# Kernel optimization log

Measured on AMD Instinct MI355X. Metric: run time of the kernel, lower is better.

Reference implementation:

```python
import jax, jax.numpy as jnp
import numpy as np

B, S, D, H = 2, 2048, 1024, 16
HD = D // H
SCALE = float(np.sqrt(HD))


def setup_inputs() -> dict:
    key = jax.random.key(0)
    ks = jax.random.split(key, 11)
    mk = lambda k, shape, s=0.02: (jax.random.normal(k, shape, dtype=jnp.float32) * s)
    query = jax.random.normal(ks[0], (B, S, D), dtype=jnp.float32)
    key_t = jax.random.normal(ks[1], (B, S, D), dtype=jnp.float32)
    value = jax.random.normal(ks[2], (B, S, D), dtype=jnp.float32)
    # causal mask: True = position is masked out
    mask = jnp.triu(jnp.ones((S, S), dtype=bool), k=1)
    return {
        "query": query, "key": key_t, "value": value, "mask": mask,
        "Wq": mk(ks[3], (D, D)), "bq": jnp.zeros((D,), jnp.float32),
        "Wk": mk(ks[4], (D, D)), "bk": jnp.zeros((D,), jnp.float32),
        "Wv": mk(ks[5], (D, D)), "bv": jnp.zeros((D,), jnp.float32),
        "Wo": mk(ks[6], (D, D)), "bo": jnp.zeros((D,), jnp.float32),
    }


def reference(query, key, value, mask, Wq, bq, Wk, bk, Wv, bv, Wo, bo):
    b = query.shape[0]
    # projections; nn.Linear computes x @ W.T + b
    q = (query @ Wq.T + bq).reshape(b, -1, H, HD).transpose(0, 2, 1, 3)  # (b,h,sq,hd)
    k = (key @ Wk.T + bk).reshape(b, -1, H, HD).transpose(0, 2, 1, 3)    # (b,h,sk,hd)
    v = (value @ Wv.T + bv).reshape(b, -1, H, HD).transpose(0, 2, 1, 3)  # (b,h,sk,hd)
    scores = jnp.einsum("bhqd,bhkd->bhqk", q, k) / SCALE
    scores = jnp.where(mask[None, None, :, :], -jnp.inf, scores)
    attn_weights = jax.nn.softmax(scores, axis=-1)  # (b,h,sq,sk)
    # dropout is identity in eval mode
    attn_out = jnp.einsum("bhqk,bhkd->bhqd", attn_weights, v)
    attn_out = attn_out.transpose(0, 2, 1, 3).reshape(b, -1, D)
    output = attn_out @ Wo.T + bo
    return output, attn_weights
```

## Files before the change

kernel.cpp:

```cpp
#include <hip/hip_runtime.h>

typedef __bf16 bf16;
typedef __bf16 bf16_8 __attribute__((ext_vector_type(8)));
typedef __bf16 bf16_4 __attribute__((ext_vector_type(4)));
typedef float f32x4 __attribute__((ext_vector_type(4)));

constexpr int kB = 2, kS = 2048, kD = 1024, kH = 16, kHD = 64;
constexpr int kM = kB * kS;
constexpr float kInvScale = 0.125f;

#define GLOBAL_AS const __attribute__((address_space(1)))
#define LDS_AS __attribute__((address_space(3)))

__device__ __forceinline__ void async_copy16(const bf16* g, bf16* l) {
  __builtin_amdgcn_global_load_lds((GLOBAL_AS unsigned int*)g,
                                   (LDS_AS unsigned int*)l, 16, 0, 0);
}

__global__ __launch_bounds__(256) void cvt4(const float4* __restrict__ src,
                                            bf16* __restrict__ dst, int n4) {
  int i = blockIdx.x * blockDim.x + threadIdx.x;
  if (i >= n4) return;
  float4 v = src[i];
  bf16_4 o = {(bf16)v.x, (bf16)v.y, (bf16)v.z, (bf16)v.w};
  *(bf16_4*)(dst + (size_t)i * 4) = o;
}

__device__ __forceinline__ void gemm_core(const bf16* __restrict__ A,
                                          const bf16* __restrict__ Bm,
                                          int m0, int n0,
                                          bf16* ldsA, bf16* ldsB,
                                          f32x4 acc[4][4]) {
  const int t = threadIdx.x;
  const int lane = t & 63, wave = t >> 6;
  const int l16 = lane & 15, quad = lane >> 4;
  const int wm = (wave >> 1) * 64, wn = (wave & 1) * 64;
  const f32x4 z4 = {0.f, 0.f, 0.f, 0.f};
#pragma unroll
  for (int i = 0; i < 4; ++i)
#pragma unroll
    for (int j = 0; j < 4; ++j) acc[i][j] = z4;

  for (int kt = 0; kt < kD; kt += 32) {
#pragma unroll
    for (int rep = 0; rep < 2; ++rep) {
      int q = t + rep * 256;
      int row = q >> 2, cc = q & 3;
      bf16* lbase_a = ldsA + (size_t)(wave * 64 + rep * 256) * 8;
      bf16* lbase_b = ldsB + (size_t)(wave * 64 + rep * 256) * 8;
      async_copy16(A + (size_t)(m0 + row) * kD + kt + cc * 8, lbase_a);
      async_copy16(Bm + (size_t)(n0 + row) * kD + kt + cc * 8, lbase_b);
    }
    __syncthreads();
    bf16_8 af[4], bfr[4];
#pragma unroll
    for (int i = 0; i < 4; ++i)
      af[i] = *(const bf16_8*)(ldsA + (wm + i * 16 + l16) * 32 + quad * 8);
#pragma unroll
    for (int j = 0; j < 4; ++j)
      bfr[j] = *(const bf16_8*)(ldsB + (wn + j * 16 + l16) * 32 + quad * 8);
#pragma unroll
    for (int i = 0; i < 4; ++i)
#pragma unroll
      for (int j = 0; j < 4; ++j)
        acc[i][j] = __builtin_amdgcn_mfma_f32_16x16x32_bf16(af[i], bfr[j],
                                                            acc[i][j], 0, 0, 0);
    __syncthreads();
  }
}

__global__ __launch_bounds__(256) void gemm_qkv(
    const bf16* __restrict__ qb, const bf16* __restrict__ kb,
    const bf16* __restrict__ vb, const bf16* __restrict__ wq,
    const bf16* __restrict__ wk, const bf16* __restrict__ wv,
    const float* __restrict__ bq, const float* __restrict__ bk,
    const float* __restrict__ bv, bf16* __restrict__ Qh,
    bf16* __restrict__ Kh, bf16* __restrict__ Vh) {
  __shared__ __align__(16) bf16 ldsA[128 * 32];
  __shared__ __align__(16) bf16 ldsB[128 * 32];
  const bf16 *A, *W;
  const float* bias;
  bf16* Out;
  int z = blockIdx.z;
  if (z == 0) { A = qb; W = wq; bias = bq; Out = Qh; }
  else if (z == 1) { A = kb; W = wk; bias = bk; Out = Kh; }
  else { A = vb; W = wv; bias = bv; Out = Vh; }
  int m0 = blockIdx.x * 128, n0 = blockIdx.y * 128;
  f32x4 acc[4][4];
  gemm_core(A, W, m0, n0, ldsA, ldsB, acc);

  const int t = threadIdx.x, lane = t & 63, wave = t >> 6;
  const int l16 = lane & 15, quad = lane >> 4;
  const int wm = (wave >> 1) * 64, wn = (wave & 1) * 64;
#pragma unroll
  for (int i = 0; i < 4; ++i)
#pragma unroll
    for (int j = 0; j < 4; ++j)
#pragma unroll
      for (int r = 0; r < 4; ++r) {
        int m = m0 + wm + i * 16 + quad * 4 + r;
        int n = n0 + wn + j * 16 + l16;
        float v = acc[i][j][r] + bias[n];
        int b = m >> 11, s = m & (kS - 1);
        int h = n >> 6, hd = n & 63;
        Out[((size_t)(b * kH + h) * kS + s) * kHD + hd] = (bf16)v;
      }
}

__global__ __launch_bounds__(256) void gemm_out(const bf16* __restrict__ AO,
                                                const bf16* __restrict__ wo,
                                                const float* __restrict__ bo,
                                                float* __restrict__ Cout) {
  __shared__ __align__(16) bf16 ldsA[128 * 32];
  __shared__ __align__(16) bf16 ldsB[128 * 32];
  int m0 = blockIdx.x * 128, n0 = blockIdx.y * 128;
  f32x4 acc[4][4];
  gemm_core(AO, wo, m0, n0, ldsA, ldsB, acc);

  const int t = threadIdx.x, lane = t & 63, wave = t >> 6;
  const int l16 = lane & 15, quad = lane >> 4;
  const int wm = (wave >> 1) * 64, wn = (wave & 1) * 64;
#pragma unroll
  for (int i = 0; i < 4; ++i)
#pragma unroll
    for (int j = 0; j < 4; ++j)
#pragma unroll
      for (int r = 0; r < 4; ++r) {
        int m = m0 + wm + i * 16 + quad * 4 + r;
        int n = n0 + wn + j * 16 + l16;
        Cout[(size_t)m * kD + n] = acc[i][j][r] + bo[n];
      }
}

__global__ __launch_bounds__(256) void attn_kernel(
    const bf16* __restrict__ Qh, const bf16* __restrict__ Kh,
    const bf16* __restrict__ Vh, float* __restrict__ attnW,
    bf16* __restrict__ AO) {
  __shared__ __align__(16) bf16 ldsK[64 * 64];
  __shared__ __align__(16) bf16 ldsVt[64 * 72];
  __shared__ __align__(16) bf16 ldsP[4 * 16 * 64];

  const int t = threadIdx.x, lane = t & 63, wave = t >> 6;
  const int l16 = lane & 15, quad = lane >> 4;
  const int qt = blockIdx.x, bh = blockIdx.y;
  const int q0 = qt * 64;

  const bf16* Qbase = Qh + ((size_t)bh * kS + q0) * kHD;
  const bf16* Kbase = Kh + (size_t)bh * kS * kHD;
  const bf16* Vbase = Vh + (size_t)bh * kS * kHD;

  bf16_8 aq0 = *(const bf16_8*)(Qbase + (wave * 16 + l16) * kHD + quad * 8);
  bf16_8 aq1 = *(const bf16_8*)(Qbase + (wave * 16 + l16) * kHD + 32 + quad * 8);

  float m_i[4], l_i[4];
#pragma unroll
  for (int r = 0; r < 4; ++r) { m_i[r] = -3.0e38f; l_i[r] = 0.f; }

  for (int kt = 0; kt <= qt; ++kt) {
    const int k0 = kt * 64;
#pragma unroll
    for (int rep = 0; rep < 2; ++rep) {
      int q = t + rep * 256;
      async_copy16(Kbase + (size_t)(k0 + (q >> 3)) * kHD + (q & 7) * 8,
                   ldsK + (size_t)(wave * 64 + rep * 256) * 8);
    }
    __syncthreads();
    f32x4 sacc[4];
#pragma unroll
    for (int j = 0; j < 4; ++j) {
      bf16_8 b0 = *(const bf16_8*)(ldsK + (j * 16 + l16) * 64 + quad * 8);
      bf16_8 b1 = *(const bf16_8*)(ldsK + (j * 16 + l16) * 64 + 32 + quad * 8);
      f32x4 z = {0.f, 0.f, 0.f, 0.f};
      z = __builtin_amdgcn_mfma_f32_16x16x32_bf16(aq0, b0, z, 0, 0, 0);
      z = __builtin_amdgcn_mfma_f32_16x16x32_bf16(aq1, b1, z, 0, 0, 0);
      sacc[j] = z;
    }
#pragma unroll
    for (int j = 0; j < 4; ++j)
#pragma unroll
      for (int r = 0; r < 4; ++r) {
        int qrow = q0 + wave * 16 + quad * 4 + r;
        int kcol = k0 + j * 16 + l16;
        float v = sacc[j][r] * kInvScale;
        sacc[j][r] = (kcol > qrow) ? -3.0e38f : v;
      }
#pragma unroll
    for (int r = 0; r < 4; ++r) {
      float mx = fmaxf(fmaxf(sacc[0][r], sacc[1][r]),
                       fmaxf(sacc[2][r], sacc[3][r]));
#pragma unroll
      for (int off = 1; off < 16; off <<= 1) mx = fmaxf(mx, __shfl_xor(mx, off, 64));
      float mnew = fmaxf(m_i[r], mx);
      float sum = 0.f;
#pragma unroll
      for (int j = 0; j < 4; ++j) sum += __expf(sacc[j][r] - mnew);
#pragma unroll
      for (int off = 1; off < 16; off <<= 1) sum += __shfl_xor(sum, off, 64);
      l_i[r] = l_i[r] * __expf(m_i[r] - mnew) + sum;
      m_i[r] = mnew;
    }
    __syncthreads();
  }

  float rl[4];
#pragma unroll
  for (int r = 0; r < 4; ++r) rl[r] = 1.0f / l_i[r];

  const f32x4 z4 = {0.f, 0.f, 0.f, 0.f};
  f32x4 oacc[4];
#pragma unroll
  for (int d = 0; d < 4; ++d) oacc[d] = z4;

  for (int kt = 0; kt < kS / 64; ++kt) {
    const int k0 = kt * 64;
    if (kt > qt) {
      const float4 zf = {0.f, 0.f, 0.f, 0.f};
      int row = t >> 2;
      float* dst = attnW + ((size_t)bh * kS + q0 + row) * kS + k0 + (t & 3) * 16;
#pragma unroll
      for (int f = 0; f < 4; ++f) ((float4*)dst)[f] = zf;
      continue;
    }
#pragma unroll
    for (int rep = 0; rep < 2; ++rep) {
      int q = t + rep * 256;
      async_copy16(Kbase + (size_t)(k0 + (q >> 3)) * kHD + (q & 7) * 8,
                   ldsK + (size_t)(wave * 64 + rep * 256) * 8);
    }
    {
      int d = t & 63, kk0 = (t >> 6) * 16;
#pragma unroll
      for (int i = 0; i < 16; ++i)
        ldsVt[(size_t)d * 72 + kk0 + i] =
            Vbase[(size_t)(k0 + kk0 + i) * kHD + d];
    }
    __syncthreads();
    f32x4 sacc[4];
#pragma unroll
    for (int j = 0; j < 4; ++j) {
      bf16_8 b0 = *(const bf16_8*)(ldsK + (j * 16 + l16) * 64 + quad * 8);
      bf16_8 b1 = *(const bf16_8*)(ldsK + (j * 16 + l16) * 64 + 32 + quad * 8);
      f32x4 z = {0.f, 0.f, 0.f, 0.f};
      z = __builtin_amdgcn_mfma_f32_16x16x32_bf16(aq0, b0, z, 0, 0, 0);
      z = __builtin_amdgcn_mfma_f32_16x16x32_bf16(aq1, b1, z, 0, 0, 0);
      sacc[j] = z;
    }
#pragma unroll
    for (int j = 0; j < 4; ++j)
#pragma unroll
      for (int r = 0; r < 4; ++r) {
        int qrl = wave * 16 + quad * 4 + r;
        int qrow = q0 + qrl;
        int kcol = k0 + j * 16 + l16;
        float v = sacc[j][r] * kInvScale;
        float p = (kcol > qrow) ? 0.f : __expf(v - m_i[r]) * rl[r];
        attnW[((size_t)bh * kS + qrow) * kS + kcol] = p;
        ldsP[(size_t)qrl * 64 + j * 16 + l16] = (bf16)p;
      }
    __syncthreads();
    bf16_8 ap0 = *(const bf16_8*)(ldsP + (wave * 16 + l16) * 64 + quad * 8);
    bf16_8 ap1 = *(const bf16_8*)(ldsP + (wave * 16 + l16) * 64 + 32 + quad * 8);
#pragma unroll
    for (int dsub = 0; dsub < 4; ++dsub) {
      bf16_8 bv0 = *(const bf16_8*)(ldsVt + (dsub * 16 + l16) * 72 + quad * 8);
      bf16_8 bv1 = *(const bf16_8*)(ldsVt + (dsub * 16 + l16) * 72 + 32 + quad * 8);
      oacc[dsub] = __builtin_amdgcn_mfma_f32_16x16x32_bf16(ap0, bv0, oacc[dsub], 0, 0, 0);
      oacc[dsub] = __builtin_amdgcn_mfma_f32_16x16x32_bf16(ap1, bv1, oacc[dsub], 0, 0, 0);
    }
    __syncthreads();
  }

  const int b = bh >> 4, h = bh & 15;
#pragma unroll
  for (int dsub = 0; dsub < 4; ++dsub)
#pragma unroll
    for (int r = 0; r < 4; ++r) {
      int qrow = q0 + wave * 16 + quad * 4 + r;
      int d = dsub * 16 + l16;
      AO[((size_t)(b * kS + qrow)) * kD + h * kHD + d] = (bf16)oacc[dsub][r];
    }
}

extern "C" void kernel_launch(void* const* d_in, const int* in_sizes, int n_in,
                              void* d_out, int out_size, void* d_ws, size_t ws_size,
                              hipStream_t stream) {
  const float* query = (const float*)d_in[0];
  const float* key_t = (const float*)d_in[1];
  const float* value = (const float*)d_in[2];
  const float* Wq = (const float*)d_in[4];
  const float* bq = (const float*)d_in[5];
  const float* Wk = (const float*)d_in[6];
  const float* bk = (const float*)d_in[7];
  const float* Wv = (const float*)d_in[8];
  const float* bv = (const float*)d_in[9];
  const float* Wo = (const float*)d_in[10];
  const float* bo = (const float*)d_in[11];

  float* out = (float*)d_out;
  float* attnW = out + (size_t)kM * kD;

  bf16* qb = (bf16*)d_ws;
  bf16* kb = qb + (size_t)kM * kD;
  bf16* vb = kb + (size_t)kM * kD;
  bf16* Qh = vb + (size_t)kM * kD;
  bf16* Kh = Qh + (size_t)kM * kD;
  bf16* Vh = Kh + (size_t)kM * kD;
  bf16* AO = Vh + (size_t)kM * kD;
  bf16* wqb = AO + (size_t)kM * kD;
  bf16* wkb = wqb + (size_t)kD * kD;
  bf16* wvb = wkb + (size_t)kD * kD;
  bf16* wob = wvb + (size_t)kD * kD;

  const int n4_x = kM * kD / 4;
  const int n4_w = kD * kD / 4;
  cvt4<<<n4_x / 256, 256, 0, stream>>>((const float4*)query, qb, n4_x);
  cvt4<<<n4_x / 256, 256, 0, stream>>>((const float4*)key_t, kb, n4_x);
  cvt4<<<n4_x / 256, 256, 0, stream>>>((const float4*)value, vb, n4_x);
  cvt4<<<n4_w / 256, 256, 0, stream>>>((const float4*)Wq, wqb, n4_w);
  cvt4<<<n4_w / 256, 256, 0, stream>>>((const float4*)Wk, wkb, n4_w);
  cvt4<<<n4_w / 256, 256, 0, stream>>>((const float4*)Wv, wvb, n4_w);
  cvt4<<<n4_w / 256, 256, 0, stream>>>((const float4*)Wo, wob, n4_w);

  gemm_qkv<<<dim3(kM / 128, kD / 128, 3), 256, 0, stream>>>(
      qb, kb, vb, wqb, wkb, wvb, bq, bk, bv, Qh, Kh, Vh);

  attn_kernel<<<dim3(kS / 64, kB * kH), 256, 0, stream>>>(Qh, Kh, Vh, attnW, AO);

  gemm_out<<<dim3(kM / 128, kD / 128), 256, 0, stream>>>(AO, wob, bo, out);
}
```

Before: 803.5 us.

## Restructure attention with double-buffered K/V, pre-transposed V and max-free softmax

Attention now double-buffers K and V tiles in LDS via async copies. V is pre-transposed by a separate kernel, replacing the scalar strided V gather. The 1/sqrt(d) scale is folded into the Q projection, and the online running max is dropped, so the first pass only accumulates exp sums. Query tiles are launched heaviest-first for causal load balance, and the seven conversion launches are merged into two. Dropping the max subtraction risks exp overflow when scores are large, and the transpose adds a kernel and extra workspace.

```diff
diff --git a/kernel.cpp b/kernel.cpp
--- a/kernel.cpp
+++ b/kernel.cpp
@@ -7,7 +7,7 @@
 
 constexpr int kB = 2, kS = 2048, kD = 1024, kH = 16, kHD = 64;
 constexpr int kM = kB * kS;
-constexpr float kInvScale = 0.125f;
+constexpr int kNT = kS / 64;
 
 #define GLOBAL_AS const __attribute__((address_space(1)))
 #define LDS_AS __attribute__((address_space(3)))
@@ -17,12 +17,33 @@
                                    (LDS_AS unsigned int*)l, 16, 0, 0);
 }
 
-__global__ __launch_bounds__(256) void cvt4(const float4* __restrict__ src,
-                                            bf16* __restrict__ dst, int n4) {
-  int i = blockIdx.x * blockDim.x + threadIdx.x;
-  if (i >= n4) return;
-  float4 v = src[i];
-  bf16_4 o = {(bf16)v.x, (bf16)v.y, (bf16)v.z, (bf16)v.w};
+__device__ __forceinline__ void barrier_lgkm() {
+  asm volatile("s_waitcnt lgkmcnt(0)\n\ts_barrier" ::: "memory");
+}
+
+__global__ __launch_bounds__(256) void cvt_act(
+    const float4* __restrict__ q, const float4* __restrict__ k,
+    const float4* __restrict__ v, bf16* __restrict__ oq,
+    bf16* __restrict__ ok, bf16* __restrict__ ov) {
+  const float4* src = blockIdx.y == 0 ? q : blockIdx.y == 1 ? k : v;
+  bf16* dst = blockIdx.y == 0 ? oq : blockIdx.y == 1 ? ok : ov;
+  int i = blockIdx.x * 256 + threadIdx.x;
+  float4 x = src[i];
+  bf16_4 o = {(bf16)x.x, (bf16)x.y, (bf16)x.z, (bf16)x.w};
+  *(bf16_4*)(dst + (size_t)i * 4) = o;
+}
+
+__global__ __launch_bounds__(256) void cvt_w(
+    const float4* __restrict__ a, const float4* __restrict__ b,
+    const float4* __restrict__ c, const float4* __restrict__ d,
+    bf16* __restrict__ oa, bf16* __restrict__ ob, bf16* __restrict__ oc,
+    bf16* __restrict__ od) {
+  int z = blockIdx.y;
+  const float4* src = z == 0 ? a : z == 1 ? b : z == 2 ? c : d;
+  bf16* dst = z == 0 ? oa : z == 1 ? ob : z == 2 ? oc : od;
+  int i = blockIdx.x * 256 + threadIdx.x;
+  float4 x = src[i];
+  bf16_4 o = {(bf16)x.x, (bf16)x.y, (bf16)x.z, (bf16)x.w};
   *(bf16_4*)(dst + (size_t)i * 4) = o;
 }
 
@@ -85,6 +106,7 @@
   if (z == 0) { A = qb; W = wq; bias = bq; Out = Qh; }
   else if (z == 1) { A = kb; W = wk; bias = bk; Out = Kh; }
   else { A = vb; W = wv; bias = bv; Out = Vh; }
+  const float scale = (z == 0) ? 0.125f : 1.0f;
   int m0 = blockIdx.x * 128, n0 = blockIdx.y * 128;
   f32x4 acc[4][4];
   gemm_core(A, W, m0, n0, ldsA, ldsB, acc);
@@ -100,11 +122,34 @@
       for (int r = 0; r < 4; ++r) {
         int m = m0 + wm + i * 16 + quad * 4 + r;
         int n = n0 + wn + j * 16 + l16;
-        float v = acc[i][j][r] + bias[n];
+        float v = (acc[i][j][r] + bias[n]) * scale;
         int b = m >> 11, s = m & (kS - 1);
         int h = n >> 6, hd = n & 63;
         Out[((size_t)(b * kH + h) * kS + s) * kHD + hd] = (bf16)v;
       }
+}
+
+__global__ __launch_bounds__(256) void transpose_v(const bf16* __restrict__ Vh,
+                                                   bf16* __restrict__ Vt) {
+  __shared__ bf16 tile[64][72];
+  const int t = threadIdx.x;
+  const int s0 = blockIdx.x * 64, bh = blockIdx.y;
+#pragma unroll
+  for (int it = 0; it < 2; ++it) {
+    int chunk = t + it * 256;
+    int s = chunk >> 3, d0 = (chunk & 7) * 8;
+    bf16_8 v = *(const bf16_8*)(Vh + ((size_t)bh * kS + s0 + s) * kHD + d0);
+#pragma unroll
+    for (int j = 0; j < 8; ++j) tile[d0 + j][s] = v[j];
+  }
+  __syncthreads();
+#pragma unroll
+  for (int it = 0; it < 2; ++it) {
+    int chunk = t + it * 256;
+    int d = chunk >> 3, c0 = (chunk & 7) * 8;
+    bf16_8 o = *(const bf16_8*)&tile[d][c0];
+    *(bf16_8*)(Vt + ((size_t)bh * kHD + d) * kS + s0 + c0) = o;
+  }
 }
 
 __global__ __launch_bounds__(256) void gemm_out(const bf16* __restrict__ AO,
@@ -134,42 +179,64 @@
 
 __global__ __launch_bounds__(256) void attn_kernel(
     const bf16* __restrict__ Qh, const bf16* __restrict__ Kh,
-    const bf16* __restrict__ Vh, float* __restrict__ attnW,
+    const bf16* __restrict__ Vt, float* __restrict__ attnW,
     bf16* __restrict__ AO) {
-  __shared__ __align__(16) bf16 ldsK[64 * 64];
-  __shared__ __align__(16) bf16 ldsVt[64 * 72];
-  __shared__ __align__(16) bf16 ldsP[4 * 16 * 64];
+  __shared__ __align__(16) bf16 ldsK[2][64 * 64];
+  __shared__ __align__(16) bf16 ldsV[2][64 * 64];
+  __shared__ __align__(16) bf16 ldsP[64 * 64];
 
   const int t = threadIdx.x, lane = t & 63, wave = t >> 6;
   const int l16 = lane & 15, quad = lane >> 4;
-  const int qt = blockIdx.x, bh = blockIdx.y;
+  const int bh = blockIdx.x;
+  const int qt = (kNT - 1) - blockIdx.y;
   const int q0 = qt * 64;
 
   const bf16* Qbase = Qh + ((size_t)bh * kS + q0) * kHD;
   const bf16* Kbase = Kh + (size_t)bh * kS * kHD;
-  const bf16* Vbase = Vh + (size_t)bh * kS * kHD;
+  const bf16* Vtbase = Vt + (size_t)bh * kHD * kS;
 
   bf16_8 aq0 = *(const bf16_8*)(Qbase + (wave * 16 + l16) * kHD + quad * 8);
   bf16_8 aq1 = *(const bf16_8*)(Qbase + (wave * 16 + l16) * kHD + 32 + quad * 8);
 
-  float m_i[4], l_i[4];
-#pragma unroll
-  for (int r = 0; r < 4; ++r) { m_i[r] = -3.0e38f; l_i[r] = 0.f; }
-
+  const int dq = t >> 3, dc = (t & 7) * 8;
+#define ISSUE_K(kt, buf)                                                      \
+  {                                                                           \
+    const int k0_ = (kt) * 64;                                                \
+    async_copy16(Kbase + (size_t)(k0_ / 64 * 64 + dq) * kHD + dc,             \
+                 &ldsK[buf][(size_t)(wave * 64) * 8]);                        \
+    async_copy16(Kbase + (size_t)(k0_ + ((t + 256) >> 3)) * kHD +             \
+                     (((t + 256) & 7) * 8),                                   \
+                 &ldsK[buf][(size_t)(wave * 64 + 256) * 8]);                  \
+  }
+#define ISSUE_V(kt, buf)                                                      \
+  {                                                                           \
+    const int k0_ = (kt) * 64;                                                \
+    async_copy16(Vtbase + (size_t)dq * kS + k0_ + dc,                         \
+                 &ldsV[buf][(size_t)(wave * 64) * 8]);                        \
+    async_copy16(Vtbase + (size_t)((t + 256) >> 3) * kS + k0_ +               \
+                     (((t + 256) & 7) * 8),                                   \
+                 &ldsV[buf][(size_t)(wave * 64 + 256) * 8]);                  \
+  }
+
+  float lp[4] = {0.f, 0.f, 0.f, 0.f};
+  {
+    const int k0f = 0;
+    async_copy16(Kbase + (size_t)(k0f + dq) * kHD + dc,
+                 &ldsK[0][(size_t)(wave * 64) * 8]);
+    async_copy16(Kbase + (size_t)(k0f + ((t + 256) >> 3)) * kHD +
+                     (((t + 256) & 7) * 8),
+                 &ldsK[0][(size_t)(wave * 64 + 256) * 8]);
+  }
   for (int kt = 0; kt <= qt; ++kt) {
+    __syncthreads();
+    if (kt < qt) ISSUE_K(kt + 1, (kt + 1) & 1);
+    const bf16* Kl = ldsK[kt & 1];
     const int k0 = kt * 64;
-#pragma unroll
-    for (int rep = 0; rep < 2; ++rep) {
-      int q = t + rep * 256;
-      async_copy16(Kbase + (size_t)(k0 + (q >> 3)) * kHD + (q & 7) * 8,
-                   ldsK + (size_t)(wave * 64 + rep * 256) * 8);
-    }
-    __syncthreads();
     f32x4 sacc[4];
 #pragma unroll
     for (int j = 0; j < 4; ++j) {
-      bf16_8 b0 = *(const bf16_8*)(ldsK + (j * 16 + l16) * 64 + quad * 8);
-      bf16_8 b1 = *(const bf16_8*)(ldsK + (j * 16 + l16) * 64 + 32 + quad * 8);
+      bf16_8 b0 = *(const bf16_8*)(Kl + (j * 16 + l16) * 64 + quad * 8);
+      bf16_8 b1 = *(const bf16_8*)(Kl + (j * 16 + l16) * 64 + 32 + quad * 8);
       f32x4 z = {0.f, 0.f, 0.f, 0.f};
       z = __builtin_amdgcn_mfma_f32_16x16x32_bf16(aq0, b0, z, 0, 0, 0);
       z = __builtin_amdgcn_mfma_f32_16x16x32_bf16(aq1, b1, z, 0, 0, 0);
@@ -181,65 +248,40 @@
       for (int r = 0; r < 4; ++r) {
         int qrow = q0 + wave * 16 + quad * 4 + r;
         int kcol = k0 + j * 16 + l16;
-        float v = sacc[j][r] * kInvScale;
-        sacc[j][r] = (kcol > qrow) ? -3.0e38f : v;
+        lp[r] += (kcol > qrow) ? 0.f : __expf(sacc[j][r]);
       }
-#pragma unroll
-    for (int r = 0; r < 4; ++r) {
-      float mx = fmaxf(fmaxf(sacc[0][r], sacc[1][r]),
-                       fmaxf(sacc[2][r], sacc[3][r]));
-#pragma unroll
-      for (int off = 1; off < 16; off <<= 1) mx = fmaxf(mx, __shfl_xor(mx, off, 64));
-      float mnew = fmaxf(m_i[r], mx);
-      float sum = 0.f;
-#pragma unroll
-      for (int j = 0; j < 4; ++j) sum += __expf(sacc[j][r] - mnew);
-#pragma unroll
-      for (int off = 1; off < 16; off <<= 1) sum += __shfl_xor(sum, off, 64);
-      l_i[r] = l_i[r] * __expf(m_i[r] - mnew) + sum;
-      m_i[r] = mnew;
-    }
-    __syncthreads();
-  }
-
+  }
   float rl[4];
 #pragma unroll
-  for (int r = 0; r < 4; ++r) rl[r] = 1.0f / l_i[r];
+  for (int r = 0; r < 4; ++r) {
+    float s = lp[r];
+#pragma unroll
+    for (int off = 1; off < 16; off <<= 1) s += __shfl_xor(s, off, 64);
+    rl[r] = 1.0f / s;
+  }
 
   const f32x4 z4 = {0.f, 0.f, 0.f, 0.f};
   f32x4 oacc[4];
 #pragma unroll
   for (int d = 0; d < 4; ++d) oacc[d] = z4;
 
-  for (int kt = 0; kt < kS / 64; ++kt) {
+  __syncthreads();
+  ISSUE_K(0, 0);
+  ISSUE_V(0, 0);
+  for (int kt = 0; kt <= qt; ++kt) {
+    __syncthreads();
+    if (kt < qt) {
+      ISSUE_K(kt + 1, (kt + 1) & 1);
+      ISSUE_V(kt + 1, (kt + 1) & 1);
+    }
+    const bf16* Kl = ldsK[kt & 1];
+    const bf16* Vl = ldsV[kt & 1];
     const int k0 = kt * 64;
-    if (kt > qt) {
-      const float4 zf = {0.f, 0.f, 0.f, 0.f};
-      int row = t >> 2;
-      float* dst = attnW + ((size_t)bh * kS + q0 + row) * kS + k0 + (t & 3) * 16;
-#pragma unroll
-      for (int f = 0; f < 4; ++f) ((float4*)dst)[f] = zf;
-      continue;
-    }
-#pragma unroll
-    for (int rep = 0; rep < 2; ++rep) {
-      int q = t + rep * 256;
-      async_copy16(Kbase + (size_t)(k0 + (q >> 3)) * kHD + (q & 7) * 8,
-                   ldsK + (size_t)(wave * 64 + rep * 256) * 8);
-    }
-    {
-      int d = t & 63, kk0 = (t >> 6) * 16;
-#pragma unroll
-      for (int i = 0; i < 16; ++i)
-        ldsVt[(size_t)d * 72 + kk0 + i] =
-            Vbase[(size_t)(k0 + kk0 + i) * kHD + d];
-    }
-    __syncthreads();
     f32x4 sacc[4];
 #pragma unroll
     for (int j = 0; j < 4; ++j) {
-      bf16_8 b0 = *(const bf16_8*)(ldsK + (j * 16 + l16) * 64 + quad * 8);
-      bf16_8 b1 = *(const bf16_8*)(ldsK + (j * 16 + l16) * 64 + 32 + quad * 8);
+      bf16_8 b0 = *(const bf16_8*)(Kl + (j * 16 + l16) * 64 + quad * 8);
+      bf16_8 b1 = *(const bf16_8*)(Kl + (j * 16 + l16) * 64 + 32 + quad * 8);
       f32x4 z = {0.f, 0.f, 0.f, 0.f};
       z = __builtin_amdgcn_mfma_f32_16x16x32_bf16(aq0, b0, z, 0, 0, 0);
       z = __builtin_amdgcn_mfma_f32_16x16x32_bf16(aq1, b1, z, 0, 0, 0);
@@ -252,22 +294,27 @@
         int qrl = wave * 16 + quad * 4 + r;
         int qrow = q0 + qrl;
         int kcol = k0 + j * 16 + l16;
-        float v = sacc[j][r] * kInvScale;
-        float p = (kcol > qrow) ? 0.f : __expf(v - m_i[r]) * rl[r];
+        float p = (kcol > qrow) ? 0.f : __expf(sacc[j][r]) * rl[r];
         attnW[((size_t)bh * kS + qrow) * kS + kcol] = p;
         ldsP[(size_t)qrl * 64 + j * 16 + l16] = (bf16)p;
       }
-    __syncthreads();
+    barrier_lgkm();
     bf16_8 ap0 = *(const bf16_8*)(ldsP + (wave * 16 + l16) * 64 + quad * 8);
     bf16_8 ap1 = *(const bf16_8*)(ldsP + (wave * 16 + l16) * 64 + 32 + quad * 8);
 #pragma unroll
     for (int dsub = 0; dsub < 4; ++dsub) {
-      bf16_8 bv0 = *(const bf16_8*)(ldsVt + (dsub * 16 + l16) * 72 + quad * 8);
-      bf16_8 bv1 = *(const bf16_8*)(ldsVt + (dsub * 16 + l16) * 72 + 32 + quad * 8);
+      bf16_8 bv0 = *(const bf16_8*)(Vl + (dsub * 16 + l16) * 64 + quad * 8);
+      bf16_8 bv1 = *(const bf16_8*)(Vl + (dsub * 16 + l16) * 64 + 32 + quad * 8);
       oacc[dsub] = __builtin_amdgcn_mfma_f32_16x16x32_bf16(ap0, bv0, oacc[dsub], 0, 0, 0);
       oacc[dsub] = __builtin_amdgcn_mfma_f32_16x16x32_bf16(ap1, bv1, oacc[dsub], 0, 0, 0);
     }
-    __syncthreads();
+  }
+  for (int kt = qt + 1; kt < kNT; ++kt) {
+    const float4 zf = {0.f, 0.f, 0.f, 0.f};
+    int row = t >> 2;
+    float* dst = attnW + ((size_t)bh * kS + q0 + row) * kS + kt * 64 + (t & 3) * 16;
+#pragma unroll
+    for (int f = 0; f < 4; ++f) ((float4*)dst)[f] = zf;
   }
 
   const int b = bh >> 4, h = bh & 15;
@@ -279,6 +326,8 @@
       int d = dsub * 16 + l16;
       AO[((size_t)(b * kS + qrow)) * kD + h * kHD + d] = (bf16)oacc[dsub][r];
     }
+#undef ISSUE_K
+#undef ISSUE_V
 }
 
 extern "C" void kernel_launch(void* const* d_in, const int* in_sizes, int n_in,
@@ -305,7 +354,8 @@
   bf16* Qh = vb + (size_t)kM * kD;
   bf16* Kh = Qh + (size_t)kM * kD;
   bf16* Vh = Kh + (size_t)kM * kD;
-  bf16* AO = Vh + (size_t)kM * kD;
+  bf16* Vtr = Vh + (size_t)kM * kD;
+  bf16* AO = Vtr + (size_t)kM * kD;
   bf16* wqb = AO + (size_t)kM * kD;
   bf16* wkb = wqb + (size_t)kD * kD;
   bf16* wvb = wkb + (size_t)kD * kD;
@@ -313,18 +363,19 @@
 
   const int n4_x = kM * kD / 4;
   const int n4_w = kD * kD / 4;
-  cvt4<<<n4_x / 256, 256, 0, stream>>>((const float4*)query, qb, n4_x);
-  cvt4<<<n4_x / 256, 256, 0, stream>>>((const float4*)key_t, kb, n4_x);
-  cvt4<<<n4_x / 256, 256, 0, stream>>>((const float4*)value, vb, n4_x);
-  cvt4<<<n4_w / 256, 256, 0, stream>>>((const float4*)Wq, wqb, n4_w);
-  cvt4<<<n4_w / 256, 256, 0, stream>>>((const float4*)Wk, wkb, n4_w);
-  cvt4<<<n4_w / 256, 256, 0, stream>>>((const float4*)Wv, wvb, n4_w);
-  cvt4<<<n4_w / 256, 256, 0, stream>>>((const float4*)Wo, wob, n4_w);
+  cvt_act<<<dim3(n4_x / 256, 3), 256, 0, stream>>>(
+      (const float4*)query, (const float4*)key_t, (const float4*)value,
+      qb, kb, vb);
+  cvt_w<<<dim3(n4_w / 256, 4), 256, 0, stream>>>(
+      (const float4*)Wq, (const float4*)Wk, (const float4*)Wv,
+      (const float4*)Wo, wqb, wkb, wvb, wob);
 
   gemm_qkv<<<dim3(kM / 128, kD / 128, 3), 256, 0, stream>>>(
       qb, kb, vb, wqb, wkb, wvb, bq, bk, bv, Qh, Kh, Vh);
 
-  attn_kernel<<<dim3(kS / 64, kB * kH), 256, 0, stream>>>(Qh, Kh, Vh, attnW, AO);
+  transpose_v<<<dim3(kS / 64, kB * kH), 256, 0, stream>>>(Vh, Vtr);
+
+  attn_kernel<<<dim3(kB * kH, kNT), 256, 0, stream>>>(Qh, Kh, Vtr, attnW, AO);
 
   gemm_out<<<dim3(kM / 128, kD / 128), 256, 0, stream>>>(AO, wob, bo, out);
 }
```

Result: faster. 765.3 us (-4.8%).
